# Performance work log

Measured on AMD Instinct MI355X. Metric: run time of the kernel, lower is better.

## Reference

```python
import jax, jax.numpy as jnp
import numpy as np
import math

B, N, M = 4, 2048, 2048
DIM_Q = DIM_K = DIM_V = 1024
H = 16

def setup_inputs() -> dict:
    key = jax.random.key(0)
    ks = jax.random.split(key, 10)
    s = 0.02
    return {
        "Q": jax.random.normal(ks[0], (B, N, DIM_Q), jnp.float32),
        "K": jax.random.normal(ks[1], (B, M, DIM_K), jnp.float32),
        "Wq": jax.random.normal(ks[2], (DIM_V, DIM_Q), jnp.float32) * s,
        "bq": jax.random.normal(ks[3], (DIM_V,), jnp.float32) * s,
        "Wk": jax.random.normal(ks[4], (DIM_V, DIM_K), jnp.float32) * s,
        "bk": jax.random.normal(ks[5], (DIM_V,), jnp.float32) * s,
        "Wv": jax.random.normal(ks[6], (DIM_V, DIM_K), jnp.float32) * s,
        "bv": jax.random.normal(ks[7], (DIM_V,), jnp.float32) * s,
        "Wo": jax.random.normal(ks[8], (DIM_V, DIM_V), jnp.float32) * s,
        "bo": jax.random.normal(ks[9], (DIM_V,), jnp.float32) * s,
    }

def reference(Q, K, Wq, bq, Wk, bk, Wv, bv, Wo, bo):
    d = DIM_V // H  # head dim
    Qp = Q @ Wq.T + bq            # [B,N,DIM_V]
    Kp = K @ Wk.T + bk            # [B,M,DIM_V]
    Vp = K @ Wv.T + bv            # [B,M,DIM_V]
    # split heads: [B,T,H,d] -> [B,H,T,d]
    Qh = Qp.reshape(B, N, H, d).transpose(0, 2, 1, 3)
    Kh = Kp.reshape(B, M, H, d).transpose(0, 2, 1, 3)
    Vh = Vp.reshape(B, M, H, d).transpose(0, 2, 1, 3)
    # NOTE: original scales by sqrt(dim_V), not sqrt(head_dim)
    scores = jnp.einsum('bhnd,bhmd->bhnm', Qh, Kh) / math.sqrt(DIM_V)
    A = jax.nn.softmax(scores, axis=-1)
    Oh = Qh + jnp.einsum('bhnm,bhmd->bhnd', A, Vh)   # residual with projected Q
    O = Oh.transpose(0, 2, 1, 3).reshape(B, N, DIM_V)
    O = O + jax.nn.relu(O @ Wo.T + bo)
    return O
```

## Files before the change

kernel.cpp:

```cpp
#include <hip/hip_runtime.h>
#include <cstddef>
#include <cstdint>


typedef unsigned short ushort_t;
typedef __attribute__((ext_vector_type(8))) short bf16x8;
typedef __attribute__((ext_vector_type(4))) float floatx4;
typedef __attribute__((ext_vector_type(8))) unsigned short us8;
typedef __attribute__((ext_vector_type(4))) unsigned short us4;

__device__ __forceinline__ ushort_t f2bf(float x) {
  union { float f; unsigned u; } v; v.f = x;
  unsigned r = v.u + 0x7FFFu + ((v.u >> 16) & 1u);
  return (ushort_t)(r >> 16);
}
__device__ __forceinline__ float bf2f(ushort_t x) {
  union { unsigned u; float f; } v; v.u = ((unsigned)x) << 16;
  return v.f;
}
__device__ __forceinline__ unsigned pk2(float a, float b) {
  union { float f; unsigned u; } x, y; x.f = a; y.f = b;
  return __builtin_amdgcn_perm(y.u + 0x8000u, x.u + 0x8000u, 0x07060302u);
}
__device__ __forceinline__ floatx4 mfma16(bf16x8 a, bf16x8 b, floatx4 c) {
  return __builtin_amdgcn_mfma_f32_16x16x32_bf16(a, b, c, 0, 0, 0);
}
__device__ __forceinline__ void gld_lds16(const void* g, void* l) {
  __builtin_amdgcn_global_load_lds(
      (const __attribute__((address_space(1))) unsigned int*)g,
      (__attribute__((address_space(3))) unsigned int*)l, 16, 0, 0);
}

__global__ void cvt4(const float* __restrict__ i0, const float* __restrict__ i1,
                     const float* __restrict__ i2, const float* __restrict__ i3,
                     ushort_t* __restrict__ o0, ushort_t* __restrict__ o1,
                     ushort_t* __restrict__ o2, ushort_t* __restrict__ o3, int n8) {
  int z = blockIdx.z;
  const float* in = z == 0 ? i0 : z == 1 ? i1 : z == 2 ? i2 : i3;
  ushort_t* out = z == 0 ? o0 : z == 1 ? o1 : z == 2 ? o2 : o3;
  int i = blockIdx.x * 256 + threadIdx.x;
  if (i < n8) {
    const float4* p = (const float4*)in + (size_t)i * 2;
    float4 a = p[0], b = p[1];
    uint4 o;
    o.x = pk2(a.x, a.y); o.y = pk2(a.z, a.w);
    o.z = pk2(b.x, b.y); o.w = pk2(b.z, b.w);
    *((uint4*)out + i) = o;
  }
}

__global__ __launch_bounds__(256, 2)
void gemm_qkv(const ushort_t* __restrict__ Qb, const ushort_t* __restrict__ Kb,
              const ushort_t* __restrict__ Wqb, const ushort_t* __restrict__ Wkb,
              const ushort_t* __restrict__ Wvb,
              const float* __restrict__ bq, const float* __restrict__ bk,
              const float* __restrict__ bv,
              ushort_t* __restrict__ Qp, ushort_t* __restrict__ Kp,
              ushort_t* __restrict__ Vt)
{
  const int Kd = 1024, Nn = 1024;
  const int z = blockIdx.z;
  const ushort_t* Ab = (z == 0) ? Qb : Kb;
  const ushort_t* Bw = (z == 0) ? Wqb : (z == 1) ? Wkb : Wvb;
  const float* bias  = (z == 0) ? bq : (z == 1) ? bk : bv;

  __shared__ __align__(16) ushort_t As[128][64];
  __shared__ __align__(16) ushort_t Bs[128][64];
  const int tid = threadIdx.x;
  const int lane = tid & 63, wave = tid >> 6;
  const int wm = (wave >> 1) * 64, wn = (wave & 1) * 64;
  const int rq = lane & 15, kg = lane >> 4;
  const int row0 = blockIdx.y * 128, col0 = blockIdx.x * 128;

  const int st_sub = lane >> 3;
  const int st_cs  = (lane & 7) ^ st_sub;

  floatx4 acc[4][4];
#pragma unroll
  for (int i = 0; i < 4; ++i)
#pragma unroll
    for (int j = 0; j < 4; ++j) acc[i][j] = (floatx4){0.f, 0.f, 0.f, 0.f};

  for (int k0 = 0; k0 < Kd; k0 += 64) {
    __syncthreads();
#pragma unroll
    for (int r = 0; r < 4; ++r) {
      int i = wave * 4 + r;
      int row = i * 8 + st_sub;
      gld_lds16(Ab + (size_t)(row0 + row) * Kd + k0 + st_cs * 8, (ushort_t*)As + i * 512);
      gld_lds16(Bw + (size_t)(col0 + row) * Kd + k0 + st_cs * 8, (ushort_t*)Bs + i * 512);
    }
    __syncthreads();
#pragma unroll
    for (int kq = 0; kq < 2; ++kq) {
      bf16x8 af[4], bfr[4];
#pragma unroll
      for (int mi = 0; mi < 4; ++mi)
        af[mi] = *(const bf16x8*)&As[wm + mi*16 + rq][((kq*4 + kg) ^ (rq & 7)) * 8];
#pragma unroll
      for (int ni = 0; ni < 4; ++ni)
        bfr[ni] = *(const bf16x8*)&Bs[wn + ni*16 + rq][((kq*4 + kg) ^ (rq & 7)) * 8];
#pragma unroll
      for (int mi = 0; mi < 4; ++mi)
#pragma unroll
        for (int ni = 0; ni < 4; ++ni)
          acc[mi][ni] = mfma16(af[mi], bfr[ni], acc[mi][ni]);
    }
  }

  float bv4[4];
#pragma unroll
  for (int ni = 0; ni < 4; ++ni) bv4[ni] = bias[col0 + wn + ni*16 + rq];

  if (z < 2) {
    ushort_t* Cb = (z == 0) ? Qp : Kp;
#pragma unroll
    for (int mi = 0; mi < 4; ++mi)
#pragma unroll
      for (int ni = 0; ni < 4; ++ni)
#pragma unroll
        for (int rr = 0; rr < 4; ++rr) {
          int row = row0 + wm + mi*16 + kg*4 + rr;
          int col = col0 + wn + ni*16 + rq;
          Cb[(size_t)row * Nn + col] = f2bf(acc[mi][ni][rr] + bv4[ni]);
        }
  } else {
#pragma unroll
    for (int mi = 0; mi < 4; ++mi)
#pragma unroll
      for (int ni = 0; ni < 4; ++ni) {
        int col = col0 + wn + ni*16 + rq;
        int r0  = row0 + wm + mi*16 + kg*4;
        us4 o = { f2bf(acc[mi][ni][0] + bv4[ni]), f2bf(acc[mi][ni][1] + bv4[ni]),
                  f2bf(acc[mi][ni][2] + bv4[ni]), f2bf(acc[mi][ni][3] + bv4[ni]) };
        *(us4*)(Vt + (size_t)col * 8192 + r0) = o;
      }
  }
}

__global__ __launch_bounds__(256, 2)
void gemm_out(const ushort_t* __restrict__ Ob, const ushort_t* __restrict__ Bw,
              const float* __restrict__ bias, float* __restrict__ Out)
{
  const int Kd = 1024, Nn = 1024;
  __shared__ __align__(16) ushort_t As[128][64];
  __shared__ __align__(16) ushort_t Bs[128][64];
  const int tid = threadIdx.x;
  const int lane = tid & 63, wave = tid >> 6;
  const int wm = (wave >> 1) * 64, wn = (wave & 1) * 64;
  const int rq = lane & 15, kg = lane >> 4;
  const int row0 = blockIdx.y * 128, col0 = blockIdx.x * 128;

  const int st_sub = lane >> 3;
  const int st_cs  = (lane & 7) ^ st_sub;

  floatx4 acc[4][4];
#pragma unroll
  for (int i = 0; i < 4; ++i)
#pragma unroll
    for (int j = 0; j < 4; ++j) acc[i][j] = (floatx4){0.f, 0.f, 0.f, 0.f};

  for (int k0 = 0; k0 < Kd; k0 += 64) {
    __syncthreads();
#pragma unroll
    for (int r = 0; r < 4; ++r) {
      int i = wave * 4 + r;
      int row = i * 8 + st_sub;
      gld_lds16(Ob + (size_t)(row0 + row) * Kd + k0 + st_cs * 8, (ushort_t*)As + i * 512);
      gld_lds16(Bw + (size_t)(col0 + row) * Kd + k0 + st_cs * 8, (ushort_t*)Bs + i * 512);
    }
    __syncthreads();
#pragma unroll
    for (int kq = 0; kq < 2; ++kq) {
      bf16x8 af[4], bfr[4];
#pragma unroll
      for (int mi = 0; mi < 4; ++mi)
        af[mi] = *(const bf16x8*)&As[wm + mi*16 + rq][((kq*4 + kg) ^ (rq & 7)) * 8];
#pragma unroll
      for (int ni = 0; ni < 4; ++ni)
        bfr[ni] = *(const bf16x8*)&Bs[wn + ni*16 + rq][((kq*4 + kg) ^ (rq & 7)) * 8];
#pragma unroll
      for (int mi = 0; mi < 4; ++mi)
#pragma unroll
        for (int ni = 0; ni < 4; ++ni)
          acc[mi][ni] = mfma16(af[mi], bfr[ni], acc[mi][ni]);
    }
  }

  float bv4[4];
#pragma unroll
  for (int ni = 0; ni < 4; ++ni) bv4[ni] = bias[col0 + wn + ni*16 + rq];
#pragma unroll
  for (int mi = 0; mi < 4; ++mi)
#pragma unroll
    for (int ni = 0; ni < 4; ++ni)
#pragma unroll
      for (int rr = 0; rr < 4; ++rr) {
        int row = row0 + wm + mi*16 + kg*4 + rr;
        int col = col0 + wn + ni*16 + rq;
        size_t idx = (size_t)row * Nn + col;
        float pre = acc[mi][ni][rr] + bv4[ni];
        Out[idx] = bf2f(Ob[idx]) + (pre > 0.f ? pre : 0.f);
      }
}

__global__ __launch_bounds__(256, 2)
void attn_kernel(const ushort_t* __restrict__ Qp,
                 const ushort_t* __restrict__ Kp,
                 const ushort_t* __restrict__ Vt,
                 ushort_t* __restrict__ Ob)
{
  const float sc2 = 0.045084439f;
  const int qt = blockIdx.x;
  const int bh = blockIdx.y;
  const int b = bh >> 4, h = bh & 15;
  const int q0 = qt * 128;

  __shared__ __align__(16) ushort_t KVs[8192];
  __shared__ __align__(16) ushort_t Ps[128][128];
  __shared__ float reds[2][128];

  const int tid = threadIdx.x, lane = tid & 63, wave = tid >> 6;
  const int whalf = wave >> 1;
  const int wsec  = wave & 1;
  const int rq = lane & 15, kg = lane >> 4;

  const size_t qkbase = (size_t)(b * 2048) * 1024 + h * 64;

#pragma unroll
  for (int r = 0; r < 4; ++r) {
    int i = wave * 4 + r;
    int row = i * 8 + (lane >> 3);
    int cs = (lane & 7) ^ (lane >> 3);
    gld_lds16(Qp + qkbase + (size_t)(q0 + row) * 1024 + cs * 8, KVs + i * 512);
  }
  __syncthreads();

  bf16x8 aq[4][2];
#pragma unroll
  for (int ni = 0; ni < 4; ++ni)
#pragma unroll
    for (int kq = 0; kq < 2; ++kq) {
      int row = wsec*64 + ni*16 + rq;
      int ch = (kq*4 + kg) ^ (rq & 7);
      bf16x8 t = *(const bf16x8*)&KVs[row * 64 + ch * 8];
#pragma unroll
      for (int e = 0; e < 8; ++e)
        t[e] = (short)f2bf(bf2f((ushort_t)t[e]) * sc2);
      aq[ni][kq] = t;
    }

  floatx4 oacc[4][2];
  float l_st[4];
#pragma unroll
  for (int mi = 0; mi < 4; ++mi) {
    oacc[mi][0] = (floatx4){0.f,0.f,0.f,0.f};
    oacc[mi][1] = (floatx4){0.f,0.f,0.f,0.f};
  }
#pragma unroll
  for (int ni = 0; ni < 4; ++ni) l_st[ni] = 0.f;

  for (int kt = 0; kt < 16; ++kt) {
    const int kv0 = kt * 128;
    __syncthreads();
#pragma unroll
    for (int r = 0; r < 4; ++r) {
      int i = wave * 4 + r;
      int row = i * 8 + (lane >> 3);
      int cs = (lane & 7) ^ (lane >> 3);
      gld_lds16(Kp + qkbase + (size_t)(kv0 + row) * 1024 + cs * 8, KVs + i * 512);
    }
    __syncthreads();

    floatx4 s[4][4];
#pragma unroll
    for (int mi = 0; mi < 4; ++mi)
#pragma unroll
      for (int ni = 0; ni < 4; ++ni) s[mi][ni] = (floatx4){0.f,0.f,0.f,0.f};
#pragma unroll
    for (int kq = 0; kq < 2; ++kq) {
      bf16x8 ak[4];
#pragma unroll
      for (int mi = 0; mi < 4; ++mi) {
        int row = whalf*64 + mi*16 + rq;
        int ch = (kq*4 + kg) ^ (rq & 7);
        ak[mi] = *(const bf16x8*)&KVs[row * 64 + ch * 8];
      }
#pragma unroll
      for (int mi = 0; mi < 4; ++mi)
#pragma unroll
        for (int ni = 0; ni < 4; ++ni)
          s[mi][ni] = mfma16(ak[mi], aq[ni][kq], s[mi][ni]);
    }
    __syncthreads();

#pragma unroll
    for (int r = 0; r < 4; ++r) {
      int i = wave * 4 + r;
      int dv = i * 4 + (lane >> 4);
      int cs = (lane & 15) ^ (dv & 7);
      gld_lds16(Vt + (size_t)(h*64 + dv) * 8192 + b * 2048 + kv0 + cs * 8,
                KVs + i * 512);
    }

#pragma unroll
    for (int mi = 0; mi < 4; ++mi)
#pragma unroll
      for (int ni = 0; ni < 4; ++ni)
#pragma unroll
        for (int rr = 0; rr < 4; ++rr)
          s[mi][ni][rr] = __builtin_amdgcn_exp2f(s[mi][ni][rr]);
#pragma unroll
    for (int ni = 0; ni < 4; ++ni) {
      float t = 0.f;
#pragma unroll
      for (int mi = 0; mi < 4; ++mi)
        t += (s[mi][ni][0] + s[mi][ni][1]) + (s[mi][ni][2] + s[mi][ni][3]);
      l_st[ni] += t;
    }
#pragma unroll
    for (int mi = 0; mi < 4; ++mi)
#pragma unroll
      for (int ni = 0; ni < 4; ++ni) {
        int q = wsec*64 + ni*16 + rq;
        int chunk = (whalf*8 + mi*2 + (kg >> 1)) ^ rq;
        int colu = chunk*8 + (kg & 1)*4;
        uint2 w;
        w.x = pk2(s[mi][ni][0], s[mi][ni][1]);
        w.y = pk2(s[mi][ni][2], s[mi][ni][3]);
        *(uint2*)&Ps[q][colu] = w;
      }
    __syncthreads();

#pragma unroll
    for (int kp = 0; kp < 4; ++kp) {
      bf16x8 pf[4], vf[2];
#pragma unroll
      for (int mi = 0; mi < 4; ++mi) {
        int row = whalf*64 + mi*16 + rq;
        int slot = (kp*4 + kg) ^ rq;
        pf[mi] = *(const bf16x8*)&Ps[row][slot * 8];
      }
#pragma unroll
      for (int n2 = 0; n2 < 2; ++n2) {
        int dv = wsec*32 + n2*16 + rq;
        int ch = (kp*4 + kg) ^ (rq & 7);
        vf[n2] = *(const bf16x8*)&KVs[dv * 128 + ch * 8];
      }
#pragma unroll
      for (int mi = 0; mi < 4; ++mi)
#pragma unroll
        for (int n2 = 0; n2 < 2; ++n2)
          oacc[mi][n2] = mfma16(pf[mi], vf[n2], oacc[mi][n2]);
    }
  }

#pragma unroll
  for (int ni = 0; ni < 4; ++ni) {
    l_st[ni] += __shfl_xor(l_st[ni], 16, 64);
    l_st[ni] += __shfl_xor(l_st[ni], 32, 64);
  }
  if (lane < 16) {
#pragma unroll
    for (int ni = 0; ni < 4; ++ni)
      reds[whalf][wsec*64 + ni*16 + rq] = l_st[ni];
  }
  __syncthreads();

#pragma unroll
  for (int mi = 0; mi < 4; ++mi)
#pragma unroll
    for (int rr = 0; rr < 4; ++rr) {
      int row = whalf*64 + mi*16 + kg*4 + rr;
      float linv = 1.0f / (reds[0][row] + reds[1][row]);
#pragma unroll
      for (int n2 = 0; n2 < 2; ++n2) {
        int col = wsec*32 + n2*16 + rq;
        size_t idx = qkbase + (size_t)(q0 + row) * 1024 + col;
        float ov = oacc[mi][n2][rr] * linv + bf2f(Qp[idx]);
        Ob[idx] = f2bf(ov);
      }
    }
}

extern "C" void kernel_launch(void* const* d_in, const int* in_sizes, int n_in,
                              void* d_out, int out_size, void* d_ws, size_t ws_size,
                              hipStream_t stream)
{
  const float* Q  = (const float*)d_in[0];
  const float* K  = (const float*)d_in[1];
  const float* Wq = (const float*)d_in[2];
  const float* bq = (const float*)d_in[3];
  const float* Wk = (const float*)d_in[4];
  const float* bk = (const float*)d_in[5];
  const float* Wv = (const float*)d_in[6];
  const float* bv = (const float*)d_in[7];
  const float* Wo = (const float*)d_in[8];
  const float* bo = (const float*)d_in[9];
  float* Out = (float*)d_out;

  ushort_t* ws = (ushort_t*)d_ws;
  const size_t E = (size_t)8192 * 1024;
  const size_t WSZ = (size_t)1024 * 1024;
  ushort_t* Qb  = ws;
  ushort_t* Kb  = ws + E;
  ushort_t* Qp  = ws + 2*E;
  ushort_t* Kp  = ws + 3*E;
  ushort_t* Vt  = ws + 4*E;
  ushort_t* Wqb = ws + 5*E;
  ushort_t* Wkb = ws + 5*E + WSZ;
  ushort_t* Wvb = ws + 5*E + 2*WSZ;
  ushort_t* Wob = ws + 5*E + 3*WSZ;
  ushort_t* Ob  = Qb;

  cvt4<<<dim3(4096, 1, 2), 256, 0, stream>>>(Q, K, K, K, Qb, Kb, Kb, Kb, 1048576);
  cvt4<<<dim3(512, 1, 4), 256, 0, stream>>>(Wq, Wk, Wv, Wo, Wqb, Wkb, Wvb, Wob, 131072);

  dim3 blk(256);
  gemm_qkv<<<dim3(8, 64, 3), blk, 0, stream>>>(Qb, Kb, Wqb, Wkb, Wvb,
                                               bq, bk, bv, Qp, Kp, Vt);
  attn_kernel<<<dim3(16, 64), blk, 0, stream>>>(Qp, Kp, Vt, Ob);
  gemm_out<<<dim3(8, 64), blk, 0, stream>>>(Ob, Wob, bo, Out);
}
```

Baseline: 333.3 us.

## Keep softmax probabilities in registers and give each wave 32 query rows

```diff
diff --git a/kernel.cpp b/kernel.cpp
--- a/kernel.cpp
+++ b/kernel.cpp
@@ -130,10 +130,11 @@
 #pragma unroll
       for (int ni = 0; ni < 4; ++ni) {
         int col = col0 + wn + ni*16 + rq;
-        int r0  = row0 + wm + mi*16 + kg*4;
+        int base32 = row0 + wm + (mi >> 1) * 32;
+        int p = kg * 8 + (mi & 1) * 4;
         us4 o = { f2bf(acc[mi][ni][0] + bv4[ni]), f2bf(acc[mi][ni][1] + bv4[ni]),
                   f2bf(acc[mi][ni][2] + bv4[ni]), f2bf(acc[mi][ni][3] + bv4[ni]) };
-        *(us4*)(Vt + (size_t)col * 8192 + r0) = o;
+        *(us4*)(Vt + (size_t)col * 8192 + base32 + p) = o;
       }
   }
 }
@@ -216,169 +217,145 @@
   const int b = bh >> 4, h = bh & 15;
   const int q0 = qt * 128;
 
-  __shared__ __align__(16) ushort_t KVs[8192];
-  __shared__ __align__(16) ushort_t Ps[128][128];
-  __shared__ float reds[2][128];
-
-  const int tid = threadIdx.x, lane = tid & 63, wave = tid >> 6;
-  const int whalf = wave >> 1;
-  const int wsec  = wave & 1;
+  __shared__ __align__(16) ushort_t Ks[8192];
+  __shared__ __align__(16) ushort_t Vs[8192];
+  __shared__ float reds[128];
+
+  const int tid = threadIdx.x, lane = tid & 63, wq = tid >> 6;
   const int rq = lane & 15, kg = lane >> 4;
 
   const size_t qkbase = (size_t)(b * 2048) * 1024 + h * 64;
 
 #pragma unroll
   for (int r = 0; r < 4; ++r) {
-    int i = wave * 4 + r;
+    int i = wq * 4 + r;
     int row = i * 8 + (lane >> 3);
     int cs = (lane & 7) ^ (lane >> 3);
-    gld_lds16(Qp + qkbase + (size_t)(q0 + row) * 1024 + cs * 8, KVs + i * 512);
+    gld_lds16(Qp + qkbase + (size_t)(q0 + row) * 1024 + cs * 8, Ks + i * 512);
   }
   __syncthreads();
 
-  bf16x8 aq[4][2];
-#pragma unroll
-  for (int ni = 0; ni < 4; ++ni)
+  bf16x8 aq[2][2];
+#pragma unroll
+  for (int ni = 0; ni < 2; ++ni)
 #pragma unroll
     for (int kq = 0; kq < 2; ++kq) {
-      int row = wsec*64 + ni*16 + rq;
-      int ch = (kq*4 + kg) ^ (rq & 7);
-      bf16x8 t = *(const bf16x8*)&KVs[row * 64 + ch * 8];
+      int row = wq * 32 + ni * 16 + rq;
+      int ch = (kq * 4 + kg) ^ (rq & 7);
+      bf16x8 t = *(const bf16x8*)&Ks[row * 64 + ch * 8];
 #pragma unroll
       for (int e = 0; e < 8; ++e)
         t[e] = (short)f2bf(bf2f((ushort_t)t[e]) * sc2);
       aq[ni][kq] = t;
     }
 
-  floatx4 oacc[4][2];
-  float l_st[4];
-#pragma unroll
-  for (int mi = 0; mi < 4; ++mi) {
-    oacc[mi][0] = (floatx4){0.f,0.f,0.f,0.f};
-    oacc[mi][1] = (floatx4){0.f,0.f,0.f,0.f};
-  }
-#pragma unroll
-  for (int ni = 0; ni < 4; ++ni) l_st[ni] = 0.f;
+  floatx4 oacc[2][4];
+  float l_st[2] = {0.f, 0.f};
+#pragma unroll
+  for (int nb = 0; nb < 2; ++nb)
+#pragma unroll
+    for (int dvb = 0; dvb < 4; ++dvb) oacc[nb][dvb] = (floatx4){0.f,0.f,0.f,0.f};
 
   for (int kt = 0; kt < 16; ++kt) {
     const int kv0 = kt * 128;
     __syncthreads();
 #pragma unroll
     for (int r = 0; r < 4; ++r) {
-      int i = wave * 4 + r;
-      int row = i * 8 + (lane >> 3);
-      int cs = (lane & 7) ^ (lane >> 3);
-      gld_lds16(Kp + qkbase + (size_t)(kv0 + row) * 1024 + cs * 8, KVs + i * 512);
-    }
-    __syncthreads();
-
-    floatx4 s[4][4];
-#pragma unroll
-    for (int mi = 0; mi < 4; ++mi)
-#pragma unroll
-      for (int ni = 0; ni < 4; ++ni) s[mi][ni] = (floatx4){0.f,0.f,0.f,0.f};
+      int i = wq * 4 + r;
+      int rowk = i * 8 + (lane >> 3);
+      int csk = (lane & 7) ^ (lane >> 3);
+      gld_lds16(Kp + qkbase + (size_t)(kv0 + rowk) * 1024 + csk * 8, Ks + i * 512);
+      int dv = i * 4 + (lane >> 4);
+      int csv = (lane & 15) ^ (dv & 7);
+      gld_lds16(Vt + (size_t)(h * 64 + dv) * 8192 + b * 2048 + kv0 + csv * 8,
+                Vs + i * 512);
+    }
+    __syncthreads();
+
+    floatx4 s[8][2];
+#pragma unroll
+    for (int mi = 0; mi < 8; ++mi) {
+      s[mi][0] = (floatx4){0.f,0.f,0.f,0.f};
+      s[mi][1] = (floatx4){0.f,0.f,0.f,0.f};
+    }
+    __builtin_amdgcn_s_setprio(1);
 #pragma unroll
     for (int kq = 0; kq < 2; ++kq) {
-      bf16x8 ak[4];
-#pragma unroll
-      for (int mi = 0; mi < 4; ++mi) {
-        int row = whalf*64 + mi*16 + rq;
-        int ch = (kq*4 + kg) ^ (rq & 7);
-        ak[mi] = *(const bf16x8*)&KVs[row * 64 + ch * 8];
-      }
-#pragma unroll
-      for (int mi = 0; mi < 4; ++mi)
-#pragma unroll
-        for (int ni = 0; ni < 4; ++ni)
+      bf16x8 ak[8];
+#pragma unroll
+      for (int mi = 0; mi < 8; ++mi)
+        ak[mi] = *(const bf16x8*)&Ks[(mi * 16 + rq) * 64 + (((kq * 4 + kg) ^ (rq & 7)) * 8)];
+#pragma unroll
+      for (int mi = 0; mi < 8; ++mi)
+#pragma unroll
+        for (int ni = 0; ni < 2; ++ni)
           s[mi][ni] = mfma16(ak[mi], aq[ni][kq], s[mi][ni]);
     }
-    __syncthreads();
-
-#pragma unroll
-    for (int r = 0; r < 4; ++r) {
-      int i = wave * 4 + r;
-      int dv = i * 4 + (lane >> 4);
-      int cs = (lane & 15) ^ (dv & 7);
-      gld_lds16(Vt + (size_t)(h*64 + dv) * 8192 + b * 2048 + kv0 + cs * 8,
-                KVs + i * 512);
-    }
-
-#pragma unroll
-    for (int mi = 0; mi < 4; ++mi)
-#pragma unroll
-      for (int ni = 0; ni < 4; ++ni)
+    __builtin_amdgcn_s_setprio(0);
+
+#pragma unroll
+    for (int mi = 0; mi < 8; ++mi)
+#pragma unroll
+      for (int ni = 0; ni < 2; ++ni)
 #pragma unroll
         for (int rr = 0; rr < 4; ++rr)
           s[mi][ni][rr] = __builtin_amdgcn_exp2f(s[mi][ni][rr]);
 #pragma unroll
-    for (int ni = 0; ni < 4; ++ni) {
+    for (int ni = 0; ni < 2; ++ni) {
       float t = 0.f;
 #pragma unroll
-      for (int mi = 0; mi < 4; ++mi)
+      for (int mi = 0; mi < 8; ++mi)
         t += (s[mi][ni][0] + s[mi][ni][1]) + (s[mi][ni][2] + s[mi][ni][3]);
       l_st[ni] += t;
     }
-#pragma unroll
-    for (int mi = 0; mi < 4; ++mi)
-#pragma unroll
-      for (int ni = 0; ni < 4; ++ni) {
-        int q = wsec*64 + ni*16 + rq;
-        int chunk = (whalf*8 + mi*2 + (kg >> 1)) ^ rq;
-        int colu = chunk*8 + (kg & 1)*4;
-        uint2 w;
-        w.x = pk2(s[mi][ni][0], s[mi][ni][1]);
-        w.y = pk2(s[mi][ni][2], s[mi][ni][3]);
-        *(uint2*)&Ps[q][colu] = w;
+
+    __builtin_amdgcn_s_setprio(1);
+#pragma unroll
+    for (int c = 0; c < 4; ++c) {
+      bf16x8 vf[4];
+#pragma unroll
+      for (int dvb = 0; dvb < 4; ++dvb) {
+        int dv = dvb * 16 + rq;
+        int ch = (c * 4 + kg) ^ (rq & 7);
+        vf[dvb] = *(const bf16x8*)&Vs[dv * 128 + ch * 8];
       }
-    __syncthreads();
-
-#pragma unroll
-    for (int kp = 0; kp < 4; ++kp) {
-      bf16x8 pf[4], vf[2];
-#pragma unroll
-      for (int mi = 0; mi < 4; ++mi) {
-        int row = whalf*64 + mi*16 + rq;
-        int slot = (kp*4 + kg) ^ rq;
-        pf[mi] = *(const bf16x8*)&Ps[row][slot * 8];
+#pragma unroll
+      for (int nb = 0; nb < 2; ++nb) {
+        union { unsigned u[4]; bf16x8 v; } pa;
+        pa.u[0] = pk2(s[2*c  ][nb][0], s[2*c  ][nb][1]);
+        pa.u[1] = pk2(s[2*c  ][nb][2], s[2*c  ][nb][3]);
+        pa.u[2] = pk2(s[2*c+1][nb][0], s[2*c+1][nb][1]);
+        pa.u[3] = pk2(s[2*c+1][nb][2], s[2*c+1][nb][3]);
+#pragma unroll
+        for (int dvb = 0; dvb < 4; ++dvb)
+          oacc[nb][dvb] = mfma16(pa.v, vf[dvb], oacc[nb][dvb]);
       }
-#pragma unroll
-      for (int n2 = 0; n2 < 2; ++n2) {
-        int dv = wsec*32 + n2*16 + rq;
-        int ch = (kp*4 + kg) ^ (rq & 7);
-        vf[n2] = *(const bf16x8*)&KVs[dv * 128 + ch * 8];
-      }
-#pragma unroll
-      for (int mi = 0; mi < 4; ++mi)
-#pragma unroll
-        for (int n2 = 0; n2 < 2; ++n2)
-          oacc[mi][n2] = mfma16(pf[mi], vf[n2], oacc[mi][n2]);
-    }
-  }
-
-#pragma unroll
-  for (int ni = 0; ni < 4; ++ni) {
+    }
+    __builtin_amdgcn_s_setprio(0);
+  }
+
+#pragma unroll
+  for (int ni = 0; ni < 2; ++ni) {
     l_st[ni] += __shfl_xor(l_st[ni], 16, 64);
     l_st[ni] += __shfl_xor(l_st[ni], 32, 64);
   }
   if (lane < 16) {
-#pragma unroll
-    for (int ni = 0; ni < 4; ++ni)
-      reds[whalf][wsec*64 + ni*16 + rq] = l_st[ni];
+    reds[wq * 32 + rq]      = l_st[0];
+    reds[wq * 32 + 16 + rq] = l_st[1];
   }
   __syncthreads();
 
 #pragma unroll
-  for (int mi = 0; mi < 4; ++mi)
+  for (int nb = 0; nb < 2; ++nb)
 #pragma unroll
     for (int rr = 0; rr < 4; ++rr) {
-      int row = whalf*64 + mi*16 + kg*4 + rr;
-      float linv = 1.0f / (reds[0][row] + reds[1][row]);
-#pragma unroll
-      for (int n2 = 0; n2 < 2; ++n2) {
-        int col = wsec*32 + n2*16 + rq;
+      int row = wq * 32 + nb * 16 + kg * 4 + rr;
+      float linv = 1.0f / reds[row];
+#pragma unroll
+      for (int dvb = 0; dvb < 4; ++dvb) {
+        int col = dvb * 16 + rq;
         size_t idx = qkbase + (size_t)(q0 + row) * 1024 + col;
-        float ov = oacc[mi][n2][rr] * linv + bf2f(Qp[idx]);
-        Ob[idx] = f2bf(ov);
+        Ob[idx] = f2bf(oacc[nb][dvb][rr] * linv + bf2f(Qp[idx]));
       }
     }
 }
```

New measurement: 313.0 us. -6.1%, faster.
